# Optimization experiments

Measured on AMD Instinct MI355X. Metric: run time of the kernel, lower is better.

Reference implementation:

```python
import jax, jax.numpy as jnp
import numpy as np
import math

DIM = 1024
HEAD = 16


def setup_inputs() -> dict:
    key = jax.random.key(0)
    k1, k2, k3, k4, k5 = jax.random.split(key, 5)
    scale = 1.0 / math.sqrt(DIM)
    return {
        "x": jax.random.normal(k1, (2, 2048, DIM), dtype=jnp.float32),
        "W_kqv": jax.random.uniform(k2, (3 * DIM, DIM), minval=-scale, maxval=scale, dtype=jnp.float32),
        "b_kqv": jax.random.uniform(k3, (3 * DIM,), minval=-scale, maxval=scale, dtype=jnp.float32),
        "W_out": jax.random.uniform(k4, (DIM, DIM), minval=-scale, maxval=scale, dtype=jnp.float32),
        "b_out": jax.random.uniform(k5, (DIM,), minval=-scale, maxval=scale, dtype=jnp.float32),
    }


def reference(x, W_kqv, b_kqv, W_out, b_out):
    b, s, h = x.shape
    head = HEAD
    d = h // head
    # fused QKV projection (torch Linear: x @ W.T + b)
    kqv = jnp.einsum("bsh,oh->bso", x, W_kqv) + b_kqv  # [b, s, 3h]
    q, k, v = jnp.split(kqv, 3, axis=-1)
    # [b, s, h] -> [b, head, s, d]
    q = q.reshape(b, s, head, d).transpose(0, 2, 1, 3)
    k = k.reshape(b, s, head, d).transpose(0, 2, 1, 3)
    v = v.reshape(b, s, head, d).transpose(0, 2, 1, 3)
    scores = jnp.einsum("bnqd,bnkd->bnqk", q, k) / jnp.sqrt(jnp.float32(d))
    attn = jax.nn.softmax(scores, axis=-1)
    ctx = jnp.einsum("bnqk,bnkd->bnqd", attn, v)  # [b, head, s, d]
    ctx = ctx.transpose(0, 2, 1, 3).reshape(b, s, h)
    return jnp.einsum("bsh,oh->bso", ctx, W_out) + b_out
```

## Files before the change

kernel.cpp:

```cpp
#include <hip/hip_runtime.h>
#include <hip/hip_bf16.h>

#define DIM   1024
#define NHEAD 16
#define HD    64
#define SEQ   2048
#define BATCH 2
#define QKV3  3072

using short8 = __attribute__((ext_vector_type(8))) short;
using f32x4  = __attribute__((ext_vector_type(4))) float;

__device__ inline short f2bf(float f) {
    union { float f; unsigned u; } x; x.f = f;
    const unsigned r = (x.u + 0x7FFFu + ((x.u >> 16) & 1u)) >> 16;
    return (short)r;
}
__device__ inline unsigned pkbf(float a, float b) {
    union { __hip_bfloat162 h; unsigned u; } cv;
    cv.h = __float22bfloat162_rn(make_float2(a, b));
    return cv.u;
}

__device__ __forceinline__ void g2l16(const void* gptr, void* ldsbase) {
    __builtin_amdgcn_global_load_lds(
        (const __attribute__((address_space(1))) unsigned int*)(unsigned long long)gptr,
        (__attribute__((address_space(3))) unsigned int*)(unsigned int)(unsigned long long)ldsbase,
        16, 0, 0);
}

__global__ __launch_bounds__(256)
void conv_bf16(const float* __restrict__ x, const float* __restrict__ wk,
               const float* __restrict__ wo,
               unsigned short* __restrict__ xb, unsigned short* __restrict__ wkb,
               unsigned short* __restrict__ wob)
{
    const int bid = blockIdx.x;
    const float* src; unsigned short* dst; size_t base;
    if (bid < 1024)      { src = x;  dst = xb;  base = (size_t)bid * 4096; }
    else if (bid < 1792) { src = wk; dst = wkb; base = (size_t)(bid - 1024) * 4096; }
    else                 { src = wo; dst = wob; base = (size_t)(bid - 1792) * 4096; }
    const size_t off = base + threadIdx.x * 16;
    const float4 f0 = *(const float4*)(src + off + 0);
    const float4 f1 = *(const float4*)(src + off + 4);
    const float4 f2 = *(const float4*)(src + off + 8);
    const float4 f3 = *(const float4*)(src + off + 12);
    uint4 o0, o1;
    o0.x = pkbf(f0.x, f0.y); o0.y = pkbf(f0.z, f0.w);
    o0.z = pkbf(f1.x, f1.y); o0.w = pkbf(f1.z, f1.w);
    o1.x = pkbf(f2.x, f2.y); o1.y = pkbf(f2.z, f2.w);
    o1.z = pkbf(f3.x, f3.y); o1.w = pkbf(f3.z, f3.w);
    *(uint4*)(dst + off + 0) = o0;
    *(uint4*)(dst + off + 8) = o1;
}

__global__ __launch_bounds__(256)
void gemm_qkv(const unsigned short* __restrict__ A, const unsigned short* __restrict__ B,
              const float* __restrict__ bias,
              unsigned short* __restrict__ qbf, unsigned short* __restrict__ kbf,
              unsigned short* __restrict__ vtbf)
{
    constexpr int BK = 32, NIT = DIM / BK;
    const int K = DIM;
    __shared__ short As[2][128 * BK];
    __shared__ short Bs[2][128 * BK];

    const int tid  = threadIdx.x;
    const int lane = tid & 63;
    const int wave = tid >> 6;
    const int quad = lane >> 4;
    const int ln   = lane & 15;
    const int wm   = (wave & 1) * 64;
    const int wn   = (wave >> 1) * 64;

    const int bid = blockIdx.x;
    const int xcd = bid & 7;
    const int t   = bid >> 3;
    const int m0  = (xcd * 4 + (t & 3)) * 128;
    const int n0  = (t >> 2) * 128;

    int srow[2], sg[2];
#pragma unroll
    for (int i = 0; i < 2; ++i) {
        const int c  = wave * 128 + i * 64 + lane;
        srow[i] = c >> 2;
        sg[i]   = (c & 3) ^ ((srow[i] >> 1) & 3);
    }

    f32x4 acc[4][4];
#pragma unroll
    for (int i = 0; i < 4; ++i)
#pragma unroll
        for (int j = 0; j < 4; ++j) acc[i][j] = (f32x4){0.f, 0.f, 0.f, 0.f};

#pragma unroll
    for (int i = 0; i < 2; ++i) {
        const int cb = wave * 128 + i * 64;
        g2l16(A + (size_t)(m0 + srow[i]) * K + sg[i] * 8, &As[0][cb * 8]);
        g2l16(B + (size_t)(n0 + srow[i]) * K + sg[i] * 8, &Bs[0][cb * 8]);
    }
    __syncthreads();

    for (int kt = 0; kt < NIT; ++kt) {
        const int p = kt & 1;
        if (kt + 1 < NIT) {
            const int kn = (kt + 1) * BK;
#pragma unroll
            for (int i = 0; i < 2; ++i) {
                const int cb = wave * 128 + i * 64;
                g2l16(A + (size_t)(m0 + srow[i]) * K + kn + sg[i] * 8, &As[1 - p][cb * 8]);
                g2l16(B + (size_t)(n0 + srow[i]) * K + kn + sg[i] * 8, &Bs[1 - p][cb * 8]);
            }
        }

        short8 a[4], b[4];
#pragma unroll
        for (int i = 0; i < 4; ++i) {
            const int row = wm + i * 16 + ln;
            const int ch  = quad ^ ((row >> 1) & 3);
            a[i] = *(const short8*)&As[p][row * BK + ch * 8];
        }
#pragma unroll
        for (int j = 0; j < 4; ++j) {
            const int row = wn + j * 16 + ln;
            const int ch  = quad ^ ((row >> 1) & 3);
            b[j] = *(const short8*)&Bs[p][row * BK + ch * 8];
        }
#pragma unroll
        for (int i = 0; i < 4; ++i)
#pragma unroll
            for (int j = 0; j < 4; ++j)
                acc[i][j] = __builtin_amdgcn_mfma_f32_16x16x32_bf16(
                    a[i], b[j], acc[i][j], 0, 0, 0);
        __syncthreads();
    }

#pragma unroll
    for (int j = 0; j < 4; ++j) {
        const int col = n0 + wn + j * 16 + ln;
        const int sel = col >> 10;
        const int c   = col & 1023;
        const int hh  = c >> 6;
        const int dd  = c & 63;
        const float bv = bias[col];
        if (sel < 2) {
            unsigned short* dst = (sel == 0) ? qbf : kbf;
            const float qs = (sel == 0) ? 0.18033688f : 1.0f;
#pragma unroll
            for (int i = 0; i < 4; ++i)
#pragma unroll
                for (int r2 = 0; r2 < 4; ++r2) {
                    const int row = m0 + wm + i * 16 + quad * 4 + r2;
                    const int bb = row >> 11, ss = row & 2047;
                    dst[((size_t)(bb * NHEAD + hh) * SEQ + ss) * HD + dd] =
                        (unsigned short)f2bf((acc[i][j][r2] + bv) * qs);
                }
        } else {
            const int row0 = m0 + wm + quad * 4;
            const int bb = row0 >> 11;
            const size_t vbase = ((size_t)(bb * NHEAD + hh) * HD + dd) * SEQ;
#pragma unroll
            for (int i = 0; i < 4; ++i) {
                const int ss0 = (row0 & 2047) + i * 16;
                uint2 pk;
                pk.x = pkbf(acc[i][j][0] + bv, acc[i][j][1] + bv);
                pk.y = pkbf(acc[i][j][2] + bv, acc[i][j][3] + bv);
                *(uint2*)&vtbf[vbase + ss0] = pk;
            }
        }
    }
}

__global__ __launch_bounds__(256)
void attn_flash_mfma(const unsigned short* __restrict__ qbf,
                     const unsigned short* __restrict__ kbf,
                     const unsigned short* __restrict__ vtbf,
                     unsigned short* __restrict__ ctxbf)
{
    constexpr int LDP = 72;
    __shared__ short Ks[2][64 * 64];
    __shared__ short Vt[2][64 * 64];
    __shared__ short Ps[128 * LDP];

    const int tid  = threadIdx.x;
    const int lane = tid & 63;
    const int wave = tid >> 6;
    const int quad = lane >> 4;
    const int ln   = lane & 15;

    const int bid = blockIdx.x;
    const int bh  = bid & 31;
    const int qt  = bid >> 5;
    const int q0  = qt * 128;
    const int b   = bh >> 4;
    const int h   = bh & 15;

    const size_t sbase = (size_t)bh * SEQ * HD;
    const size_t vbase = (size_t)bh * HD * SEQ;

    int srw[2], scg[2];
#pragma unroll
    for (int it = 0; it < 2; ++it) {
        const int ch = tid + it * 256;
        srw[it] = ch >> 3;
        scg[it] = (ch & 7) ^ (srw[it] & 7);
    }

#pragma unroll
    for (int it = 0; it < 4; ++it) {
        const int ch = tid + it * 256;
        const int r  = ch >> 3;
        const int cc = ch & 7;
        *(short8*)&Ps[r * LDP + cc * 8] =
            *(const short8*)&qbf[sbase + (size_t)(q0 + r) * HD + cc * 8];
    }
#pragma unroll
    for (int it = 0; it < 2; ++it) {
        const int cb = tid + it * 256;
        g2l16(kbf + sbase + (size_t)srw[it] * HD + scg[it] * 8, &Ks[0][cb * 8]);
        g2l16(vtbf + vbase + (size_t)srw[it] * SEQ + scg[it] * 8, &Vt[0][cb * 8]);
    }
    __syncthreads();

    short8 qf[2][2];
#pragma unroll
    for (int sm = 0; sm < 2; ++sm)
#pragma unroll
        for (int kc = 0; kc < 2; ++kc)
            qf[sm][kc] = *(const short8*)&Ps[(wave * 32 + sm * 16 + ln) * LDP + kc * 32 + quad * 8];

    f32x4 O[2][4];
#pragma unroll
    for (int sm = 0; sm < 2; ++sm)
#pragma unroll
        for (int dj = 0; dj < 4; ++dj) O[sm][dj] = (f32x4){0.f, 0.f, 0.f, 0.f};
    f32x4 lacc[2];
    lacc[0] = (f32x4){0.f, 0.f, 0.f, 0.f};
    lacc[1] = (f32x4){0.f, 0.f, 0.f, 0.f};

    short8 vone;
#pragma unroll
    for (int t = 0; t < 8; ++t) vone[t] = (short)0x3F80;

    for (int kt = 0; kt < SEQ / 64; ++kt) {
        const int p = kt & 1;
        if (kt + 1 < SEQ / 64) {
            const int k0n = (kt + 1) * 64;
#pragma unroll
            for (int it = 0; it < 2; ++it) {
                const int cb = tid + it * 256;
                g2l16(kbf + sbase + (size_t)(k0n + srw[it]) * HD + scg[it] * 8,
                      &Ks[1 - p][cb * 8]);
                g2l16(vtbf + vbase + (size_t)srw[it] * SEQ + k0n + scg[it] * 8,
                      &Vt[1 - p][cb * 8]);
            }
        }

        f32x4 st[2][4];
#pragma unroll
        for (int j = 0; j < 4; ++j) {
            const int row = j * 16 + ln;
            const int c0 = quad ^ (row & 7);
            const int c1 = (4 + quad) ^ (row & 7);
            const short8 kf0 = *(const short8*)&Ks[p][row * 64 + c0 * 8];
            const short8 kf1 = *(const short8*)&Ks[p][row * 64 + c1 * 8];
#pragma unroll
            for (int sm = 0; sm < 2; ++sm) {
                f32x4 tt = __builtin_amdgcn_mfma_f32_16x16x32_bf16(
                    kf0, qf[sm][0], (f32x4){0.f, 0.f, 0.f, 0.f}, 0, 0, 0);
                st[sm][j] = __builtin_amdgcn_mfma_f32_16x16x32_bf16(
                    kf1, qf[sm][1], tt, 0, 0, 0);
            }
        }

#pragma unroll
        for (int sm = 0; sm < 2; ++sm)
#pragma unroll
            for (int j = 0; j < 4; ++j) {
                const float p0 = __builtin_amdgcn_exp2f(st[sm][j][0]);
                const float p1 = __builtin_amdgcn_exp2f(st[sm][j][1]);
                const float p2 = __builtin_amdgcn_exp2f(st[sm][j][2]);
                const float p3 = __builtin_amdgcn_exp2f(st[sm][j][3]);
                uint2 pk;
                pk.x = pkbf(p0, p1);
                pk.y = pkbf(p2, p3);
                *(uint2*)&Ps[(wave * 32 + sm * 16 + ln) * LDP + j * 16 + quad * 4] = pk;
            }

#pragma unroll
        for (int kc = 0; kc < 2; ++kc) {
            const short8 pf0 = *(const short8*)&Ps[(wave * 32 + ln) * LDP + kc * 32 + quad * 8];
            const short8 pf1 = *(const short8*)&Ps[(wave * 32 + 16 + ln) * LDP + kc * 32 + quad * 8];
            lacc[0] = __builtin_amdgcn_mfma_f32_16x16x32_bf16(pf0, vone, lacc[0], 0, 0, 0);
            lacc[1] = __builtin_amdgcn_mfma_f32_16x16x32_bf16(pf1, vone, lacc[1], 0, 0, 0);
#pragma unroll
            for (int dj = 0; dj < 4; ++dj) {
                const int row = dj * 16 + ln;
                const int cg  = (kc * 4 + quad) ^ (row & 7);
                const short8 vf = *(const short8*)&Vt[p][row * 64 + cg * 8];
                O[0][dj] = __builtin_amdgcn_mfma_f32_16x16x32_bf16(pf0, vf, O[0][dj], 0, 0, 0);
                O[1][dj] = __builtin_amdgcn_mfma_f32_16x16x32_bf16(pf1, vf, O[1][dj], 0, 0, 0);
            }
        }
        __syncthreads();
    }

#pragma unroll
    for (int sm = 0; sm < 2; ++sm)
#pragma unroll
        for (int r2 = 0; r2 < 4; ++r2) {
            const float inv = 1.0f / lacc[sm][r2];
            const int row = b * SEQ + q0 + wave * 32 + sm * 16 + quad * 4 + r2;
#pragma unroll
            for (int dj = 0; dj < 4; ++dj)
                ctxbf[(size_t)row * DIM + h * HD + dj * 16 + ln] =
                    (unsigned short)f2bf(O[sm][dj][r2] * inv);
        }
}

__global__ __launch_bounds__(256)
void gemm_out(const unsigned short* __restrict__ A, const unsigned short* __restrict__ B,
              const float* __restrict__ bias, float* __restrict__ C)
{
    constexpr int BK = 32, NIT = DIM / BK;
    const int K = DIM, N = DIM;
    __shared__ short As[2][128 * BK];
    __shared__ short Bs[2][64 * BK];

    const int tid  = threadIdx.x;
    const int lane = tid & 63;
    const int wave = tid >> 6;
    const int quad = lane >> 4;
    const int ln   = lane & 15;
    const int wm   = (wave & 1) * 64;
    const int wn   = (wave >> 1) * 32;

    const int bid = blockIdx.x;
    const int xcd = bid & 7;
    const int t   = bid >> 3;
    const int m0  = (xcd * 4 + (t & 3)) * 128;
    const int n0  = (t >> 2) * 64;

    int srow[2], sg[2];
#pragma unroll
    for (int i = 0; i < 2; ++i) {
        const int c  = wave * 128 + i * 64 + lane;
        srow[i] = c >> 2;
        sg[i]   = (c & 3) ^ ((srow[i] >> 1) & 3);
    }
    const int cB  = wave * 64 + lane;
    const int brow = cB >> 2;
    const int bg   = (cB & 3) ^ ((brow >> 1) & 3);

    f32x4 acc[4][2];
#pragma unroll
    for (int i = 0; i < 4; ++i)
#pragma unroll
        for (int j = 0; j < 2; ++j) acc[i][j] = (f32x4){0.f, 0.f, 0.f, 0.f};

#pragma unroll
    for (int i = 0; i < 2; ++i)
        g2l16(A + (size_t)(m0 + srow[i]) * K + sg[i] * 8,
              &As[0][(wave * 128 + i * 64) * 8]);
    g2l16(B + (size_t)(n0 + brow) * K + bg * 8, &Bs[0][(wave * 64) * 8]);
    __syncthreads();

    for (int kt = 0; kt < NIT; ++kt) {
        const int p = kt & 1;
        if (kt + 1 < NIT) {
            const int kn = (kt + 1) * BK;
#pragma unroll
            for (int i = 0; i < 2; ++i)
                g2l16(A + (size_t)(m0 + srow[i]) * K + kn + sg[i] * 8,
                      &As[1 - p][(wave * 128 + i * 64) * 8]);
            g2l16(B + (size_t)(n0 + brow) * K + kn + bg * 8, &Bs[1 - p][(wave * 64) * 8]);
        }

        short8 a[4], b[2];
#pragma unroll
        for (int i = 0; i < 4; ++i) {
            const int row = wm + i * 16 + ln;
            const int ch  = quad ^ ((row >> 1) & 3);
            a[i] = *(const short8*)&As[p][row * BK + ch * 8];
        }
#pragma unroll
        for (int j = 0; j < 2; ++j) {
            const int row = wn + j * 16 + ln;
            const int ch  = quad ^ ((row >> 1) & 3);
            b[j] = *(const short8*)&Bs[p][row * BK + ch * 8];
        }
#pragma unroll
        for (int i = 0; i < 4; ++i)
#pragma unroll
            for (int j = 0; j < 2; ++j)
                acc[i][j] = __builtin_amdgcn_mfma_f32_16x16x32_bf16(
                    a[i], b[j], acc[i][j], 0, 0, 0);
        __syncthreads();
    }

#pragma unroll
    for (int j = 0; j < 2; ++j) {
        const int col = n0 + wn + j * 16 + ln;
        const float bv = bias[col];
#pragma unroll
        for (int i = 0; i < 4; ++i)
#pragma unroll
            for (int r2 = 0; r2 < 4; ++r2) {
                const int row = m0 + wm + i * 16 + quad * 4 + r2;
                C[(size_t)row * N + col] = acc[i][j][r2] + bv;
            }
    }
}

extern "C" void kernel_launch(void* const* d_in, const int* in_sizes, int n_in,
                              void* d_out, int out_size, void* d_ws, size_t ws_size,
                              hipStream_t stream)
{
    const float* x     = (const float*)d_in[0];
    const float* W_kqv = (const float*)d_in[1];
    const float* b_kqv = (const float*)d_in[2];
    const float* W_out = (const float*)d_in[3];
    const float* b_out = (const float*)d_in[4];
    float* out = (float*)d_out;

    char* w = (char*)d_ws;
    unsigned short* qbf   = (unsigned short*)w;  w += (size_t)BATCH * NHEAD * SEQ * HD * 2;
    unsigned short* kbf   = (unsigned short*)w;  w += (size_t)BATCH * NHEAD * SEQ * HD * 2;
    unsigned short* vtbf  = (unsigned short*)w;  w += (size_t)BATCH * NHEAD * HD * SEQ * 2;
    unsigned short* ctxbf = (unsigned short*)w;  w += (size_t)BATCH * SEQ * DIM * 2;
    unsigned short* xb    = (unsigned short*)w;  w += (size_t)BATCH * SEQ * DIM * 2;
    unsigned short* wkb   = (unsigned short*)w;  w += (size_t)QKV3 * DIM * 2;
    unsigned short* wob   = (unsigned short*)w;

    dim3 blk(256);

    conv_bf16<<<dim3(2048), blk, 0, stream>>>(x, W_kqv, W_out, xb, wkb, wob);

    gemm_qkv<<<dim3(768), blk, 0, stream>>>(xb, wkb, b_kqv, qbf, kbf, vtbf);

    attn_flash_mfma<<<dim3(512), blk, 0, stream>>>(qbf, kbf, vtbf, ctxbf);

    gemm_out<<<dim3(512), blk, 0, stream>>>(ctxbf, wob, b_out, out);
}
```

Measured before the change: 190.7 us.

## Keep softmax probabilities in registers via permlane swaps instead of LDS round-trip

The P tile is no longer written to shared memory and read back in MFMA operand layout. The layout change is now done in registers with permlane32_swap and permlane16_swap on the packed bf16 values. Q fragments are also loaded straight from global memory into registers, so the Ps shared buffer goes away entirely. This removes LDS traffic and cuts shared-memory use, which may raise occupancy, in exchange for extra cross-lane permute instructions. Correctness depends on the permute sequence exactly matching the MFMA A-operand layout.

```diff
diff --git a/kernel.cpp b/kernel.cpp
--- a/kernel.cpp
+++ b/kernel.cpp
@@ -177,10 +177,8 @@
                      const unsigned short* __restrict__ vtbf,
                      unsigned short* __restrict__ ctxbf)
 {
-    constexpr int LDP = 72;
     __shared__ short Ks[2][64 * 64];
     __shared__ short Vt[2][64 * 64];
-    __shared__ short Ps[128 * LDP];
 
     const int tid  = threadIdx.x;
     const int lane = tid & 63;
@@ -206,14 +204,14 @@
         scg[it] = (ch & 7) ^ (srw[it] & 7);
     }
 
-#pragma unroll
-    for (int it = 0; it < 4; ++it) {
-        const int ch = tid + it * 256;
-        const int r  = ch >> 3;
-        const int cc = ch & 7;
-        *(short8*)&Ps[r * LDP + cc * 8] =
-            *(const short8*)&qbf[sbase + (size_t)(q0 + r) * HD + cc * 8];
-    }
+    short8 qf[2][2];
+#pragma unroll
+    for (int sm = 0; sm < 2; ++sm)
+#pragma unroll
+        for (int kc = 0; kc < 2; ++kc)
+            qf[sm][kc] = *(const short8*)&qbf[sbase +
+                (size_t)(q0 + wave * 32 + sm * 16 + ln) * HD + kc * 32 + quad * 8];
+
 #pragma unroll
     for (int it = 0; it < 2; ++it) {
         const int cb = tid + it * 256;
@@ -221,13 +219,6 @@
         g2l16(vtbf + vbase + (size_t)srw[it] * SEQ + scg[it] * 8, &Vt[0][cb * 8]);
     }
     __syncthreads();
-
-    short8 qf[2][2];
-#pragma unroll
-    for (int sm = 0; sm < 2; ++sm)
-#pragma unroll
-        for (int kc = 0; kc < 2; ++kc)
-            qf[sm][kc] = *(const short8*)&Ps[(wave * 32 + sm * 16 + ln) * LDP + kc * 32 + quad * 8];
 
     f32x4 O[2][4];
 #pragma unroll
@@ -273,33 +264,45 @@
             }
         }
 
-#pragma unroll
-        for (int sm = 0; sm < 2; ++sm)
+        short8 pf[2][2];
+#pragma unroll
+        for (int sm = 0; sm < 2; ++sm) {
+            unsigned lo[4], hi[4];
 #pragma unroll
             for (int j = 0; j < 4; ++j) {
-                const float p0 = __builtin_amdgcn_exp2f(st[sm][j][0]);
-                const float p1 = __builtin_amdgcn_exp2f(st[sm][j][1]);
-                const float p2 = __builtin_amdgcn_exp2f(st[sm][j][2]);
-                const float p3 = __builtin_amdgcn_exp2f(st[sm][j][3]);
-                uint2 pk;
-                pk.x = pkbf(p0, p1);
-                pk.y = pkbf(p2, p3);
-                *(uint2*)&Ps[(wave * 32 + sm * 16 + ln) * LDP + j * 16 + quad * 4] = pk;
-            }
+                const float e0 = __builtin_amdgcn_exp2f(st[sm][j][0]);
+                const float e1 = __builtin_amdgcn_exp2f(st[sm][j][1]);
+                const float e2 = __builtin_amdgcn_exp2f(st[sm][j][2]);
+                const float e3 = __builtin_amdgcn_exp2f(st[sm][j][3]);
+                lo[j] = pkbf(e0, e1);
+                hi[j] = pkbf(e2, e3);
+            }
+#pragma unroll
+            for (int kc = 0; kc < 2; ++kc) {
+                auto sa = __builtin_amdgcn_permlane32_swap(lo[2 * kc], lo[2 * kc + 1], false, false);
+                auto sb = __builtin_amdgcn_permlane32_swap(hi[2 * kc], hi[2 * kc + 1], false, false);
+                auto ua = __builtin_amdgcn_permlane16_swap(sa[0], sa[1], false, false);
+                auto ub = __builtin_amdgcn_permlane16_swap(sb[0], sb[1], false, false);
+                union { unsigned u[4]; short8 s; } cv;
+                cv.u[0] = ua[0];
+                cv.u[1] = ub[0];
+                cv.u[2] = ua[1];
+                cv.u[3] = ub[1];
+                pf[sm][kc] = cv.s;
+            }
+        }
 
 #pragma unroll
         for (int kc = 0; kc < 2; ++kc) {
-            const short8 pf0 = *(const short8*)&Ps[(wave * 32 + ln) * LDP + kc * 32 + quad * 8];
-            const short8 pf1 = *(const short8*)&Ps[(wave * 32 + 16 + ln) * LDP + kc * 32 + quad * 8];
-            lacc[0] = __builtin_amdgcn_mfma_f32_16x16x32_bf16(pf0, vone, lacc[0], 0, 0, 0);
-            lacc[1] = __builtin_amdgcn_mfma_f32_16x16x32_bf16(pf1, vone, lacc[1], 0, 0, 0);
+            lacc[0] = __builtin_amdgcn_mfma_f32_16x16x32_bf16(pf[0][kc], vone, lacc[0], 0, 0, 0);
+            lacc[1] = __builtin_amdgcn_mfma_f32_16x16x32_bf16(pf[1][kc], vone, lacc[1], 0, 0, 0);
 #pragma unroll
             for (int dj = 0; dj < 4; ++dj) {
                 const int row = dj * 16 + ln;
                 const int cg  = (kc * 4 + quad) ^ (row & 7);
                 const short8 vf = *(const short8*)&Vt[p][row * 64 + cg * 8];
-                O[0][dj] = __builtin_amdgcn_mfma_f32_16x16x32_bf16(pf0, vf, O[0][dj], 0, 0, 0);
-                O[1][dj] = __builtin_amdgcn_mfma_f32_16x16x32_bf16(pf1, vf, O[1][dj], 0, 0, 0);
+                O[0][dj] = __builtin_amdgcn_mfma_f32_16x16x32_bf16(pf[0][kc], vf, O[0][dj], 0, 0, 0);
+                O[1][dj] = __builtin_amdgcn_mfma_f32_16x16x32_bf16(pf[1][kc], vf, O[1][dj], 0, 0, 0);
             }
         }
         __syncthreads();
```

Result: faster. 186.1 us (-2.4%).
